# Performance work log

Hardware: AMD Instinct MI355X
Metric: run time of the kernel (lower is better)

## Reference

```python
import jax, jax.numpy as jnp
from jax import lax
import numpy as np

B, H, W, C = 64, 224, 224, 3
OH, OW = 224, 224
EPS = 1e-3  # keras BatchNormalization default epsilon
FLAT = 52 * 52 * 10  # after conv7(valid)->pool2->conv5(valid)->pool2 on 224x224


def setup_inputs() -> dict:
    key = jax.random.key(0)
    ks = jax.random.split(key, 6)
    return {
        "x": jax.random.normal(ks[0], (B, H, W, C), jnp.float32),
        "c1_w": jax.random.normal(ks[1], (7, 7, C, 8), jnp.float32) * 0.05,
        "c1_b": jnp.zeros((8,), jnp.float32),
        "g1": jnp.ones((8,), jnp.float32),
        "b1": jnp.zeros((8,), jnp.float32),
        "m1": jnp.zeros((8,), jnp.float32),
        "v1": jnp.ones((8,), jnp.float32),
        "c2_w": jax.random.normal(ks[2], (5, 5, 8, 10), jnp.float32) * 0.05,
        "c2_b": jnp.zeros((10,), jnp.float32),
        "g2": jnp.ones((10,), jnp.float32),
        "b2": jnp.zeros((10,), jnp.float32),
        "m2": jnp.zeros((10,), jnp.float32),
        "v2": jnp.ones((10,), jnp.float32),
        "d1_w": jax.random.normal(ks[3], (FLAT, 32), jnp.float32) * 0.01,
        "d1_b": jnp.zeros((32,), jnp.float32),
        "d2_w": jax.random.normal(ks[4], (32, 6), jnp.float32) * 0.01,
        "d2_b": jnp.array([1.0, 0.0, 0.0, 0.0, 1.0, 0.0], jnp.float32),  # identity affine
    }


def _conv(x, w, b):
    return lax.conv_general_dilated(x, w, (1, 1), 'VALID',
                                    dimension_numbers=('NHWC', 'HWIO', 'NHWC')) + b


def _maxpool(x):
    return lax.reduce_window(x, -jnp.inf, lax.max, (1, 2, 2, 1), (1, 2, 2, 1), 'VALID')


def _bn(x, g, b, m, v):
    # inference-mode batchnorm: gamma*(x-mean)/sqrt(var+eps)+beta
    return (x - m) * lax.rsqrt(v + EPS) * g + b


def _bilinear(img, px, py):
    # img: [H,W,C]; px,py: [OH,OW] pixel-space sample coords; zero fill outside
    x0 = jnp.floor(px).astype(jnp.int32)
    y0 = jnp.floor(py).astype(jnp.int32)

    def gather(yi, xi):
        valid = (yi >= 0) & (yi < H) & (xi >= 0) & (xi < W)
        v = img[jnp.clip(yi, 0, H - 1), jnp.clip(xi, 0, W - 1)]  # [OH,OW,C]
        return v * valid[..., None]

    wx = (px - x0)[..., None]
    wy = (py - y0)[..., None]
    return (gather(y0, x0) * (1 - wx) * (1 - wy)
            + gather(y0, x0 + 1) * wx * (1 - wy)
            + gather(y0 + 1, x0) * (1 - wx) * wy
            + gather(y0 + 1, x0 + 1) * wx * wy)


def reference(x, c1_w, c1_b, g1, b1, m1, v1, c2_w, c2_b, g2, b2, m2, v2,
              d1_w, d1_b, d2_w, d2_b):
    # localization network
    h = _maxpool(_bn(jax.nn.relu(_conv(x, c1_w, c1_b)), g1, b1, m1, v1))
    h = _maxpool(_bn(jax.nn.relu(_conv(h, c2_w, c2_b)), g2, b2, m2, v2))
    h = h.reshape(h.shape[0], -1)                      # [B, FLAT]
    h = jax.nn.relu(h @ d1_w + d1_b)                   # [B, 32]
    theta = (h @ d2_w + d2_b).reshape(-1, 2, 3)        # [B, 2, 3]

    # normalized homogeneous grid [N,3] with N = OH*OW
    xs = jnp.linspace(-1.0, 1.0, OW)
    ys = jnp.linspace(-1.0, 1.0, OH)
    xg, yg = jnp.meshgrid(xs, ys)
    grid = jnp.stack([xg.ravel(), yg.ravel(), jnp.ones(OH * OW, jnp.float32)], axis=-1)

    coords = jnp.einsum('bij,nj->bni', theta, grid)    # [B, N, 2]
    px = ((coords[..., 0] + 1.0) * 0.5 * (W - 1)).reshape(-1, OH, OW)
    py = ((coords[..., 1] + 1.0) * 0.5 * (H - 1)).reshape(-1, OH, OW)
    return jax.vmap(_bilinear)(x, px, py)              # [B, OH, OW, C]
```

## Files before the change

kernel.cpp:

```cpp
#include <hip/hip_runtime.h>
#include <hip/hip_bf16.h>


#define BB 64
#define HH 224
#define WW 224
#define CC 3

__global__ __launch_bounds__(256) void k_conv1(
    const float* __restrict__ x, const float* __restrict__ w,
    const float* __restrict__ bias, const float* __restrict__ g,
    const float* __restrict__ bt, const float* __restrict__ m,
    const float* __restrict__ v, float* __restrict__ out) {
  __shared__ float s_in[38 * 114];
  __shared__ float s_w[7 * 7 * 3 * 8];
  __shared__ float s_scale[8], s_shift[8], s_bias[8];
  const int tid = threadIdx.x;
  const int bx = blockIdx.x, by = blockIdx.y, b = blockIdx.z;

  for (int f = tid; f < 1176; f += 256) s_w[f] = w[f];
  if (tid < 8) {
    float sc = g[tid] * rsqrtf(v[tid] + 1e-3f);
    s_scale[tid] = sc;
    s_shift[tid] = bt[tid] - m[tid] * sc;
    s_bias[tid] = bias[tid];
  }
  const int iy0 = by * 32, ix0 = bx * 32;
  const float* xb = x + (size_t)b * HH * WW * CC;
  for (int f = tid; f < 38 * 114; f += 256) {
    int r = f / 114, rem = f - r * 114;
    int q = rem / 3, c = rem - q * 3;
    int gy = iy0 + r; if (gy > 223) gy = 223;
    int gc = ix0 + q; if (gc > 223) gc = 223;
    s_in[f] = xb[(gy * 224 + gc) * 3 + c];
  }
  __syncthreads();

  const int pyl = tid >> 4, pxl = tid & 15;
  const int ly = 2 * pyl, lx = 2 * pxl;
  float acc[4][8];
#pragma unroll
  for (int i = 0; i < 4; i++)
#pragma unroll
    for (int j = 0; j < 8; j++) acc[i][j] = 0.f;

#pragma unroll 1
  for (int ky = 0; ky < 7; ky++) {
#pragma unroll
    for (int kx = 0; kx < 7; kx++) {
#pragma unroll
      for (int ci = 0; ci < 3; ci++) {
        const int r0 = (ly + ky) * 114 + (lx + kx) * 3 + ci;
        const int r1 = r0 + 114;
        float i00 = s_in[r0], i01 = s_in[r0 + 3];
        float i10 = s_in[r1], i11 = s_in[r1 + 3];
        const float* wp = &s_w[((ky * 7 + kx) * 3 + ci) * 8];
#pragma unroll
        for (int co = 0; co < 8; co++) {
          float wv = wp[co];
          acc[0][co] = fmaf(i00, wv, acc[0][co]);
          acc[1][co] = fmaf(i01, wv, acc[1][co]);
          acc[2][co] = fmaf(i10, wv, acc[2][co]);
          acc[3][co] = fmaf(i11, wv, acc[3][co]);
        }
      }
    }
  }

  const int py = by * 16 + pyl, px = bx * 16 + pxl;
  if (py < 109 && px < 109) {
    float res[8];
#pragma unroll
    for (int co = 0; co < 8; co++) {
      float sc = s_scale[co], sh = s_shift[co], bs = s_bias[co];
      float a0 = fmaxf(acc[0][co] + bs, 0.f) * sc + sh;
      float a1 = fmaxf(acc[1][co] + bs, 0.f) * sc + sh;
      float a2 = fmaxf(acc[2][co] + bs, 0.f) * sc + sh;
      float a3 = fmaxf(acc[3][co] + bs, 0.f) * sc + sh;
      res[co] = fmaxf(fmaxf(a0, a1), fmaxf(a2, a3));
    }
    float4* op = (float4*)&out[(((size_t)b * 109 + py) * 109 + px) * 8];
    op[0] = make_float4(res[0], res[1], res[2], res[3]);
    op[1] = make_float4(res[4], res[5], res[6], res[7]);
  }
}

__global__ __launch_bounds__(256) void k_conv2(
    const float* __restrict__ in, const float* __restrict__ w,
    const float* __restrict__ bias, const float* __restrict__ g,
    const float* __restrict__ bt, const float* __restrict__ m,
    const float* __restrict__ v, float* __restrict__ out) {
  __shared__ float s_in[36 * 288];
  __shared__ float s_w[5 * 5 * 8 * 10];
  __shared__ float s_scale[10], s_shift[10], s_bias[10];
  const int tid = threadIdx.x;
  const int bx = blockIdx.x, by = blockIdx.y, b = blockIdx.z;

  for (int f = tid; f < 2000; f += 256) s_w[f] = w[f];
  if (tid < 10) {
    float sc = g[tid] * rsqrtf(v[tid] + 1e-3f);
    s_scale[tid] = sc;
    s_shift[tid] = bt[tid] - m[tid] * sc;
    s_bias[tid] = bias[tid];
  }
  const int iy0 = by * 32, ix0 = bx * 32;
  const float* ib = in + (size_t)b * 109 * 109 * 8;
  for (int f = tid; f < 36 * 288; f += 256) {
    int r = f / 288, rem = f - r * 288;
    int q = rem >> 3, c = rem & 7;
    int gy = iy0 + r; if (gy > 108) gy = 108;
    int gc = ix0 + q; if (gc > 108) gc = 108;
    s_in[f] = ib[(gy * 109 + gc) * 8 + c];
  }
  __syncthreads();

  const int pyl = tid >> 4, pxl = tid & 15;
  const int ly = 2 * pyl, lx = 2 * pxl;
  float acc[4][10];
#pragma unroll
  for (int i = 0; i < 4; i++)
#pragma unroll
    for (int j = 0; j < 10; j++) acc[i][j] = 0.f;

#pragma unroll 1
  for (int ky = 0; ky < 5; ky++) {
#pragma unroll
    for (int kx = 0; kx < 5; kx++) {
#pragma unroll
      for (int ci = 0; ci < 8; ci++) {
        const int r0 = (ly + ky) * 288 + (lx + kx) * 8 + ci;
        const int r1 = r0 + 288;
        float i00 = s_in[r0], i01 = s_in[r0 + 8];
        float i10 = s_in[r1], i11 = s_in[r1 + 8];
        const float* wp = &s_w[((ky * 5 + kx) * 8 + ci) * 10];
#pragma unroll
        for (int co = 0; co < 10; co++) {
          float wv = wp[co];
          acc[0][co] = fmaf(i00, wv, acc[0][co]);
          acc[1][co] = fmaf(i01, wv, acc[1][co]);
          acc[2][co] = fmaf(i10, wv, acc[2][co]);
          acc[3][co] = fmaf(i11, wv, acc[3][co]);
        }
      }
    }
  }

  const int py = by * 16 + pyl, px = bx * 16 + pxl;
  if (py < 52 && px < 52) {
    float res[10];
#pragma unroll
    for (int co = 0; co < 10; co++) {
      float sc = s_scale[co], sh = s_shift[co], bs = s_bias[co];
      float a0 = fmaxf(acc[0][co] + bs, 0.f) * sc + sh;
      float a1 = fmaxf(acc[1][co] + bs, 0.f) * sc + sh;
      float a2 = fmaxf(acc[2][co] + bs, 0.f) * sc + sh;
      float a3 = fmaxf(acc[3][co] + bs, 0.f) * sc + sh;
      res[co] = fmaxf(fmaxf(a0, a1), fmaxf(a2, a3));
    }
    float* op = &out[(((size_t)b * 52 + py) * 52 + px) * 10];
    float2* op2 = (float2*)op;
#pragma unroll
    for (int i = 0; i < 5; i++)
      op2[i] = make_float2(res[2 * i], res[2 * i + 1]);
  }
}

#define NCHUNK 212
#define KC 128
__global__ __launch_bounds__(256) void k_fc1(
    const float* __restrict__ act, const float* __restrict__ w,
    float* __restrict__ partial) {
  __shared__ float s_w[KC * 32];
  __shared__ float s_a[64 * KC];
  const int tid = threadIdx.x;
  const int chunk = blockIdx.x;
  const int k0 = chunk * KC;
  for (int f = tid; f < KC * 32; f += 256) {
    int k = k0 + (f >> 5);
    s_w[f] = (k < 27040) ? w[(size_t)k0 * 32 + f] : 0.f;
  }
  for (int f = tid; f < 64 * KC; f += 256) {
    int bb = f >> 7, j = f & (KC - 1);
    int k = k0 + j;
    s_a[f] = (k < 27040) ? act[(size_t)bb * 27040 + k] : 0.f;
  }
  __syncthreads();
  const int o = tid & 31, bh = tid >> 5;
  float sums[8];
#pragma unroll
  for (int i = 0; i < 8; i++) sums[i] = 0.f;
#pragma unroll 1
  for (int j = 0; j < KC; j++) {
    float wv = s_w[j * 32 + o];
#pragma unroll
    for (int i = 0; i < 8; i++)
      sums[i] = fmaf(s_a[(i * 8 + bh) * KC + j], wv, sums[i]);
  }
#pragma unroll
  for (int i = 0; i < 8; i++)
    partial[(size_t)chunk * 2048 + i * 256 + tid] = sums[i];
}

__global__ __launch_bounds__(64) void k_fc2(
    const float* __restrict__ partial, const float* __restrict__ d1b,
    const float* __restrict__ d2w, const float* __restrict__ d2b,
    float* __restrict__ theta) {
  const int b = blockIdx.x;
  const int t = threadIdx.x;
  const int o = t & 31, half = t >> 5;
  float s = 0.f;
  const int c0 = half * (NCHUNK / 2), c1 = c0 + (NCHUNK / 2);
  for (int c = c0; c < c1; c++)
    s += partial[(size_t)c * 2048 + b * 32 + o];
  s += __shfl_down(s, 32);
  __shared__ float s_h[32];
  if (t < 32) s_h[o] = fmaxf(s + d1b[o], 0.f);
  __syncthreads();
  if (t < 6) {
    float th = d2b[t];
#pragma unroll
    for (int o2 = 0; o2 < 32; o2++) th = fmaf(s_h[o2], d2w[o2 * 6 + t], th);
    theta[b * 6 + t] = th;
  }
}

__global__ __launch_bounds__(256) void k_sample(
    const float* __restrict__ x, const float* __restrict__ theta,
    float* __restrict__ out) {
  const int b = blockIdx.y;
  __shared__ float th[6];
  if (threadIdx.x < 6) th[threadIdx.x] = theta[b * 6 + threadIdx.x];
  __syncthreads();
  const int t = blockIdx.x * 256 + threadIdx.x;
  const int oy = t / 224, ox = t - oy * 224;
  const float xn = -1.f + (2.f / 223.f) * (float)ox;
  const float yn = -1.f + (2.f / 223.f) * (float)oy;
  const float cx = th[0] * xn + th[1] * yn + th[2];
  const float cy = th[3] * xn + th[4] * yn + th[5];
  const float px = (cx + 1.f) * 0.5f * 223.f;
  const float py = (cy + 1.f) * 0.5f * 223.f;
  const float x0f = floorf(px), y0f = floorf(py);
  const int x0 = (int)x0f, y0 = (int)y0f;
  const float wx = px - x0f, wy = py - y0f;
  const float* xb = x + (size_t)b * HH * WW * CC;
  float a0 = 0.f, a1 = 0.f, a2 = 0.f;
#pragma unroll
  for (int dy = 0; dy < 2; dy++) {
    const int yi = y0 + dy;
    const bool vy = (yi >= 0) && (yi < 224);
    const int yc = yi < 0 ? 0 : (yi > 223 ? 223 : yi);
    const float wyv = dy ? wy : 1.f - wy;
#pragma unroll
    for (int dx = 0; dx < 2; dx++) {
      const int xi = x0 + dx;
      const bool vx = (xi >= 0) && (xi < 224);
      const int xc = xi < 0 ? 0 : (xi > 223 ? 223 : xi);
      const float wv = wyv * (dx ? wx : 1.f - wx) * ((vx && vy) ? 1.f : 0.f);
      const float* p = &xb[(yc * 224 + xc) * 3];
      a0 = fmaf(p[0], wv, a0);
      a1 = fmaf(p[1], wv, a1);
      a2 = fmaf(p[2], wv, a2);
    }
  }
  float* op = &out[((size_t)b * 50176 + t) * 3];
  op[0] = a0; op[1] = a1; op[2] = a2;
}

extern "C" void kernel_launch(void* const* d_in, const int* in_sizes, int n_in,
                              void* d_out, int out_size, void* d_ws, size_t ws_size,
                              hipStream_t stream) {
  const float* x    = (const float*)d_in[0];
  const float* c1w  = (const float*)d_in[1];
  const float* c1b  = (const float*)d_in[2];
  const float* g1   = (const float*)d_in[3];
  const float* b1   = (const float*)d_in[4];
  const float* m1   = (const float*)d_in[5];
  const float* v1   = (const float*)d_in[6];
  const float* c2w  = (const float*)d_in[7];
  const float* c2b  = (const float*)d_in[8];
  const float* g2   = (const float*)d_in[9];
  const float* b2   = (const float*)d_in[10];
  const float* m2   = (const float*)d_in[11];
  const float* v2   = (const float*)d_in[12];
  const float* d1w  = (const float*)d_in[13];
  const float* d1b  = (const float*)d_in[14];
  const float* d2w  = (const float*)d_in[15];
  const float* d2b  = (const float*)d_in[16];
  float* out = (float*)d_out;

  float* ws = (float*)d_ws;
  float* p1    = ws;
  float* p2    = p1 + 6083072;
  float* part  = p2 + 1730560;
  float* theta = part + (size_t)NCHUNK * 2048;

  k_conv1<<<dim3(7, 7, 64), 256, 0, stream>>>(x, c1w, c1b, g1, b1, m1, v1, p1);
  k_conv2<<<dim3(4, 4, 64), 256, 0, stream>>>(p1, c2w, c2b, g2, b2, m2, v2, p2);
  k_fc1<<<NCHUNK, 256, 0, stream>>>(p2, d1w, part);
  k_fc2<<<64, 64, 0, stream>>>(part, d1b, d2w, d2b, theta);
  k_sample<<<dim3(196, 64), 256, 0, stream>>>(x, theta, out);
}
```

Baseline: 308.7 us.

## Use planar smem layout, row-reuse register tiling, and scalar weight loads in convs

Both conv kernels now store the input tile in shared memory as channel-planar [ci][row][col], load each input row into registers once with float2 reads, and reuse it for both output rows of the 2x2 pool window. Weights are read straight from global memory with uniform indices, which should compile to scalar loads, instead of being staged through shared memory. The intermediate activation between conv1 and conv2 switches to a channel-major [C][B][H][W] layout. The aim is fewer LDS reads and bank conflicts per FMA, at the cost of strided per-channel global stores in conv1 and more registers.

```diff
diff --git a/kernel.cpp b/kernel.cpp
--- a/kernel.cpp
+++ b/kernel.cpp
@@ -2,23 +2,19 @@
 #include <hip/hip_bf16.h>
 
 
-#define BB 64
-#define HH 224
-#define WW 224
-#define CC 3
+#define NCHUNK 212
+#define KC 128
 
 __global__ __launch_bounds__(256) void k_conv1(
     const float* __restrict__ x, const float* __restrict__ w,
     const float* __restrict__ bias, const float* __restrict__ g,
     const float* __restrict__ bt, const float* __restrict__ m,
     const float* __restrict__ v, float* __restrict__ out) {
-  __shared__ float s_in[38 * 114];
-  __shared__ float s_w[7 * 7 * 3 * 8];
+  __shared__ float s_in[3][38][40];
   __shared__ float s_scale[8], s_shift[8], s_bias[8];
   const int tid = threadIdx.x;
   const int bx = blockIdx.x, by = blockIdx.y, b = blockIdx.z;
 
-  for (int f = tid; f < 1176; f += 256) s_w[f] = w[f];
   if (tid < 8) {
     float sc = g[tid] * rsqrtf(v[tid] + 1e-3f);
     s_scale[tid] = sc;
@@ -26,13 +22,13 @@
     s_bias[tid] = bias[tid];
   }
   const int iy0 = by * 32, ix0 = bx * 32;
-  const float* xb = x + (size_t)b * HH * WW * CC;
+  const float* xb = x + (size_t)b * 224 * 224 * 3;
   for (int f = tid; f < 38 * 114; f += 256) {
     int r = f / 114, rem = f - r * 114;
     int q = rem / 3, c = rem - q * 3;
     int gy = iy0 + r; if (gy > 223) gy = 223;
     int gc = ix0 + q; if (gc > 223) gc = 223;
-    s_in[f] = xb[(gy * 224 + gc) * 3 + c];
+    s_in[c][r][q] = xb[(gy * 224 + gc) * 3 + c];
   }
   __syncthreads();
 
@@ -45,31 +41,49 @@
     for (int j = 0; j < 8; j++) acc[i][j] = 0.f;
 
 #pragma unroll 1
-  for (int ky = 0; ky < 7; ky++) {
-#pragma unroll
-    for (int kx = 0; kx < 7; kx++) {
-#pragma unroll
-      for (int ci = 0; ci < 3; ci++) {
-        const int r0 = (ly + ky) * 114 + (lx + kx) * 3 + ci;
-        const int r1 = r0 + 114;
-        float i00 = s_in[r0], i01 = s_in[r0 + 3];
-        float i10 = s_in[r1], i11 = s_in[r1 + 3];
-        const float* wp = &s_w[((ky * 7 + kx) * 3 + ci) * 8];
-#pragma unroll
-        for (int co = 0; co < 8; co++) {
-          float wv = wp[co];
-          acc[0][co] = fmaf(i00, wv, acc[0][co]);
-          acc[1][co] = fmaf(i01, wv, acc[1][co]);
-          acc[2][co] = fmaf(i10, wv, acc[2][co]);
-          acc[3][co] = fmaf(i11, wv, acc[3][co]);
+  for (int r = 0; r < 8; ++r) {
+    float row[3][8];
+#pragma unroll
+    for (int ci = 0; ci < 3; ci++)
+#pragma unroll
+      for (int j = 0; j < 4; j++) {
+        float2 t = *(const float2*)&s_in[ci][ly + r][lx + 2 * j];
+        row[ci][2 * j] = t.x; row[ci][2 * j + 1] = t.y;
+      }
+    if (r < 7) {
+#pragma unroll
+      for (int kx = 0; kx < 7; kx++)
+#pragma unroll
+        for (int ci = 0; ci < 3; ci++) {
+          const float* wp = &w[((r * 7 + kx) * 3 + ci) * 8];
+          float i0 = row[ci][kx], i1 = row[ci][kx + 1];
+#pragma unroll
+          for (int co = 0; co < 8; co++) {
+            float wv = wp[co];
+            acc[0][co] = fmaf(i0, wv, acc[0][co]);
+            acc[1][co] = fmaf(i1, wv, acc[1][co]);
+          }
         }
-      }
+    }
+    if (r >= 1) {
+#pragma unroll
+      for (int kx = 0; kx < 7; kx++)
+#pragma unroll
+        for (int ci = 0; ci < 3; ci++) {
+          const float* wp = &w[(((r - 1) * 7 + kx) * 3 + ci) * 8];
+          float i0 = row[ci][kx], i1 = row[ci][kx + 1];
+#pragma unroll
+          for (int co = 0; co < 8; co++) {
+            float wv = wp[co];
+            acc[2][co] = fmaf(i0, wv, acc[2][co]);
+            acc[3][co] = fmaf(i1, wv, acc[3][co]);
+          }
+        }
     }
   }
 
   const int py = by * 16 + pyl, px = bx * 16 + pxl;
   if (py < 109 && px < 109) {
-    float res[8];
 #pragma unroll
     for (int co = 0; co < 8; co++) {
       float sc = s_scale[co], sh = s_shift[co], bs = s_bias[co];
@@ -77,11 +91,9 @@
       float a1 = fmaxf(acc[1][co] + bs, 0.f) * sc + sh;
       float a2 = fmaxf(acc[2][co] + bs, 0.f) * sc + sh;
       float a3 = fmaxf(acc[3][co] + bs, 0.f) * sc + sh;
-      res[co] = fmaxf(fmaxf(a0, a1), fmaxf(a2, a3));
-    }
-    float4* op = (float4*)&out[(((size_t)b * 109 + py) * 109 + px) * 8];
-    op[0] = make_float4(res[0], res[1], res[2], res[3]);
-    op[1] = make_float4(res[4], res[5], res[6], res[7]);
+      out[(((size_t)co * 64 + b) * 109 + py) * 109 + px] =
+          fmaxf(fmaxf(a0, a1), fmaxf(a2, a3));
+    }
   }
 }
 
@@ -90,13 +102,11 @@
     const float* __restrict__ bias, const float* __restrict__ g,
     const float* __restrict__ bt, const float* __restrict__ m,
     const float* __restrict__ v, float* __restrict__ out) {
-  __shared__ float s_in[36 * 288];
-  __shared__ float s_w[5 * 5 * 8 * 10];
+  __shared__ float s_in[8][36][40];
   __shared__ float s_scale[10], s_shift[10], s_bias[10];
   const int tid = threadIdx.x;
   const int bx = blockIdx.x, by = blockIdx.y, b = blockIdx.z;
 
-  for (int f = tid; f < 2000; f += 256) s_w[f] = w[f];
   if (tid < 10) {
     float sc = g[tid] * rsqrtf(v[tid] + 1e-3f);
     s_scale[tid] = sc;
@@ -104,13 +114,12 @@
     s_bias[tid] = bias[tid];
   }
   const int iy0 = by * 32, ix0 = bx * 32;
-  const float* ib = in + (size_t)b * 109 * 109 * 8;
-  for (int f = tid; f < 36 * 288; f += 256) {
-    int r = f / 288, rem = f - r * 288;
-    int q = rem >> 3, c = rem & 7;
+  for (int f = tid; f < 8 * 36 * 36; f += 256) {
+    int ci = f / 1296, rem = f - ci * 1296;
+    int r = rem / 36, q = rem - r * 36;
     int gy = iy0 + r; if (gy > 108) gy = 108;
     int gc = ix0 + q; if (gc > 108) gc = 108;
-    s_in[f] = ib[(gy * 109 + gc) * 8 + c];
+    s_in[ci][r][q] = in[(((size_t)ci * 64 + b) * 109 + gy) * 109 + gc];
   }
   __syncthreads();
 
@@ -123,25 +132,44 @@
     for (int j = 0; j < 10; j++) acc[i][j] = 0.f;
 
 #pragma unroll 1
-  for (int ky = 0; ky < 5; ky++) {
-#pragma unroll
-    for (int kx = 0; kx < 5; kx++) {
-#pragma unroll
-      for (int ci = 0; ci < 8; ci++) {
-        const int r0 = (ly + ky) * 288 + (lx + kx) * 8 + ci;
-        const int r1 = r0 + 288;
-        float i00 = s_in[r0], i01 = s_in[r0 + 8];
-        float i10 = s_in[r1], i11 = s_in[r1 + 8];
-        const float* wp = &s_w[((ky * 5 + kx) * 8 + ci) * 10];
-#pragma unroll
-        for (int co = 0; co < 10; co++) {
-          float wv = wp[co];
-          acc[0][co] = fmaf(i00, wv, acc[0][co]);
-          acc[1][co] = fmaf(i01, wv, acc[1][co]);
-          acc[2][co] = fmaf(i10, wv, acc[2][co]);
-          acc[3][co] = fmaf(i11, wv, acc[3][co]);
+  for (int r = 0; r < 6; ++r) {
+    float row[8][6];
+#pragma unroll
+    for (int ci = 0; ci < 8; ci++)
+#pragma unroll
+      for (int j = 0; j < 3; j++) {
+        float2 t = *(const float2*)&s_in[ci][ly + r][lx + 2 * j];
+        row[ci][2 * j] = t.x; row[ci][2 * j + 1] = t.y;
+      }
+    if (r < 5) {
+#pragma unroll
+      for (int kx = 0; kx < 5; kx++)
+#pragma unroll
+        for (int ci = 0; ci < 8; ci++) {
+          const float* wp = &w[((r * 5 + kx) * 8 + ci) * 10];
+          float i0 = row[ci][kx], i1 = row[ci][kx + 1];
+#pragma unroll
+          for (int co = 0; co < 10; co++) {
+            float wv = wp[co];
+            acc[0][co] = fmaf(i0, wv, acc[0][co]);
+            acc[1][co] = fmaf(i1, wv, acc[1][co]);
+          }
         }
-      }
+    }
+    if (r >= 1) {
+#pragma unroll
+      for (int kx = 0; kx < 5; kx++)
+#pragma unroll
+        for (int ci = 0; ci < 8; ci++) {
+          const float* wp = &w[(((r - 1) * 5 + kx) * 8 + ci) * 10];
+          float i0 = row[ci][kx], i1 = row[ci][kx + 1];
+#pragma unroll
+          for (int co = 0; co < 10; co++) {
+            float wv = wp[co];
+            acc[2][co] = fmaf(i0, wv, acc[2][co]);
+            acc[3][co] = fmaf(i1, wv, acc[3][co]);
+          }
+        }
     }
   }
 
@@ -157,16 +185,13 @@
       float a3 = fmaxf(acc[3][co] + bs, 0.f) * sc + sh;
       res[co] = fmaxf(fmaxf(a0, a1), fmaxf(a2, a3));
     }
-    float* op = &out[(((size_t)b * 52 + py) * 52 + px) * 10];
-    float2* op2 = (float2*)op;
+    float2* op2 = (float2*)&out[(((size_t)b * 52 + py) * 52 + px) * 10];
 #pragma unroll
     for (int i = 0; i < 5; i++)
       op2[i] = make_float2(res[2 * i], res[2 * i + 1]);
   }
 }
 
-#define NCHUNK 212
-#define KC 128
 __global__ __launch_bounds__(256) void k_fc1(
     const float* __restrict__ act, const float* __restrict__ w,
     float* __restrict__ partial) {
@@ -242,7 +267,7 @@
   const float x0f = floorf(px), y0f = floorf(py);
   const int x0 = (int)x0f, y0 = (int)y0f;
   const float wx = px - x0f, wy = py - y0f;
-  const float* xb = x + (size_t)b * HH * WW * CC;
+  const float* xb = x + (size_t)b * 224 * 224 * 3;
   float a0 = 0.f, a1 = 0.f, a2 = 0.f;
 #pragma unroll
   for (int dy = 0; dy < 2; dy++) {
```

Measured after the change: 316.9 us. 1.03x slower.
